# Kernel tuning notes

Hardware: AMD Instinct MI355X
Metric: run time of the kernel (lower is better)

The kernel has to match this reference:

```python
import jax, jax.numpy as jnp
import numpy as np

N = 50000          # nodes
E = 1600000        # edges (before self-loops)
DIN = 128
HEADS = (8, 8, 4)
FEATS = (16, 16, 16)
NEG_SLOPE = 0.2


def setup_inputs() -> dict:
    key = jax.random.key(0)
    ks = jax.random.split(key, 2 + 4 * 3)
    inp = {
        "X": jax.random.normal(ks[0], (N, DIN), dtype=jnp.float32),
        "A": jax.random.randint(ks[1], (2, E), 0, N, dtype=jnp.int32),
    }
    in_dims = [DIN, HEADS[0] * FEATS[0], HEADS[1] * FEATS[1]]
    k = 2
    for i, (h, f) in enumerate(zip(HEADS, FEATS)):
        din = in_dims[i]
        concat = i + 1 < len(HEADS)
        inp[f"W{i+1}"] = jax.random.normal(ks[k], (din, h * f), dtype=jnp.float32) / np.float32(np.sqrt(din)); k += 1
        inp[f"as{i+1}"] = jax.random.normal(ks[k], (h, f), dtype=jnp.float32) * 0.1; k += 1
        inp[f"ad{i+1}"] = jax.random.normal(ks[k], (h, f), dtype=jnp.float32) * 0.1; k += 1
        inp[f"b{i+1}"] = jnp.zeros((h * f if concat else f,), dtype=jnp.float32); k += 1
    return inp


def _gat_conv(x, src, dst, W, a_src, a_dst, b, concat):
    # PyG-style GATConv (eval mode, self-loops already in src/dst)
    H, F = a_src.shape
    h = (x @ W).reshape(-1, H, F)                     # [N, H, F]
    e = jax.nn.leaky_relu((h * a_src).sum(-1)[src] + (h * a_dst).sum(-1)[dst], NEG_SLOPE)  # [Etot, H]
    m = jax.ops.segment_max(e, dst, num_segments=N)   # segment softmax over dst neighborhoods
    ex = jnp.exp(e - m[dst])
    s = jax.ops.segment_sum(ex, dst, num_segments=N)
    alpha = ex / (s[dst] + 1e-16)                     # [Etot, H]
    out = jax.ops.segment_sum(h[src] * alpha[:, :, None], dst, num_segments=N)  # [N, H, F]
    out = out.reshape(N, H * F) if concat else out.mean(axis=1)
    return out + b


def reference(X, A, W1, as1, ad1, b1, W2, as2, ad2, b2, W3, as3, ad3, b3):
    loops = jnp.arange(N, dtype=A.dtype)              # GATConv default add_self_loops=True
    src = jnp.concatenate([A[0], loops])
    dst = jnp.concatenate([A[1], loops])
    x = jax.nn.relu(_gat_conv(X, src, dst, W1, as1, ad1, b1, True))
    x = jax.nn.relu(_gat_conv(x, src, dst, W2, as2, ad2, b2, True))
    return _gat_conv(x, src, dst, W3, as3, ad3, b3, False)
```

## Files before the change

kernel.cpp:

```cpp
#include <hip/hip_runtime.h>
#include <hip/hip_bf16.h>

#define NN 50000
#define EE 1600000
#define DIN 128

#define BKT_SHIFT 6
#define NB ((NN + 63) >> 6)
#define BSLACK 2688
#define CHUNK 4096

typedef _Float16 half_t;
typedef __attribute__((ext_vector_type(2))) _Float16 half2_t;
typedef __attribute__((ext_vector_type(4))) _Float16 half4_t;
typedef __attribute__((ext_vector_type(8))) _Float16 half8_t;
typedef __attribute__((ext_vector_type(4))) float float4_t;

__device__ __forceinline__ void split_write(half_t* __restrict__ bh, half_t* __restrict__ bl,
                                            int idx, float v) {
    half_t h = (half_t)v;
    bh[idx] = h;
    bl[idx] = (half_t)(v - (float)h);
}

__device__ __forceinline__ void build_bt(const float* __restrict__ W,
                                         const float* __restrict__ as,
                                         const float* __restrict__ ad,
                                         half_t* __restrict__ Bh, half_t* __restrict__ Bl,
                                         int elem, int NCOL, int H) {
    int r = elem >> 7, k = elem & 127;
    float v;
    if (r < NCOL) {
        v = W[k * NCOL + r];
    } else {
        int j = r - NCOL;
        v = 0.f;
        if (j < 8) {
            if (j < H) {
                float s = 0.f;
#pragma unroll
                for (int f = 0; f < 16; ++f) s += W[k * NCOL + j * 16 + f] * as[j * 16 + f];
                v = s;
            }
        } else {
            int hh = j - 8;
            if (hh < H) {
                float s = 0.f;
#pragma unroll
                for (int f = 0; f < 16; ++f) s += W[k * NCOL + hh * 16 + f] * ad[hh * 16 + f];
                v = s;
            }
        }
    }
    split_write(Bh, Bl, r * 128 + k, v);
}

#define T1 (144 * 128)
#define T3 (80 * 128)
__global__ __launch_bounds__(256) void prep_kernel(
    const float* __restrict__ W1, const float* __restrict__ W2, const float* __restrict__ W3,
    const float* __restrict__ as1, const float* __restrict__ ad1,
    const float* __restrict__ as2, const float* __restrict__ ad2,
    const float* __restrict__ as3, const float* __restrict__ ad3,
    half_t* __restrict__ B1h, half_t* __restrict__ B1l,
    half_t* __restrict__ B2h, half_t* __restrict__ B2l,
    half_t* __restrict__ B3h, half_t* __restrict__ B3l,
    int* __restrict__ gcursor) {
    int id = blockIdx.x * 256 + threadIdx.x;
    if (id < T1) {
        build_bt(W1, as1, ad1, B1h, B1l, id, 128, 8);
    } else if (id < 2 * T1) {
        build_bt(W2, as2, ad2, B2h, B2l, id - T1, 128, 8);
    } else if (id < 2 * T1 + T3) {
        build_bt(W3, as3, ad3, B3h, B3l, id - 2 * T1, 64, 4);
    } else {
        int i = id - (2 * T1 + T3);
        if (i < NB) gcursor[i] = 0;
    }
}

__global__ __launch_bounds__(256) void bin_kernel(const int* __restrict__ A,
                                                  int* __restrict__ gcursor,
                                                  int* __restrict__ binned, int e, int n) {
    __shared__ int lcount[NB];
    __shared__ int lbase[NB];
    int chunk0 = blockIdx.x * CHUNK;
    int cend = chunk0 + CHUNK;
    if (cend > e + n) cend = e + n;
    for (int i = threadIdx.x; i < NB; i += 256) lcount[i] = 0;
    __syncthreads();
    int sreg[16], dreg[16];
#pragma unroll
    for (int l = 0; l < 16; ++l) {
        int i = chunk0 + l * 256 + threadIdx.x;
        if (i < cend) {
            if (i < e) { sreg[l] = A[i]; dreg[l] = A[e + i]; }
            else       { sreg[l] = dreg[l] = i - e; }
            atomicAdd(&lcount[dreg[l] >> BKT_SHIFT], 1);
        } else {
            dreg[l] = -1;
        }
    }
    __syncthreads();
    for (int b = threadIdx.x; b < NB; b += 256) {
        int c = lcount[b];
        lbase[b] = c ? atomicAdd(&gcursor[b], c) : 0;
        lcount[b] = 0;
    }
    __syncthreads();
#pragma unroll
    for (int l = 0; l < 16; ++l) {
        if (dreg[l] >= 0) {
            int bkt = dreg[l] >> BKT_SHIFT;
            int pos = lbase[bkt] + atomicAdd(&lcount[bkt], 1);
            if (pos < BSLACK)
                binned[(size_t)bkt * BSLACK + pos] = (sreg[l] << 6) | (dreg[l] & 63);
        }
    }
}

__global__ __launch_bounds__(256) void fine_scatter(const int* __restrict__ binned,
                                                    const int* __restrict__ gcursor,
                                                    int* __restrict__ begE,
                                                    int* __restrict__ endE,
                                                    int* __restrict__ csr) {
    __shared__ int lc[64];
    __shared__ int scur[64];
    int b = blockIdx.x;
    int node0 = b << BKT_SHIFT;
    int cnt = gcursor[b];
    if (cnt > BSLACK) cnt = BSLACK;
    const int* bp = binned + (size_t)b * BSLACK;
    if (threadIdx.x < 64) lc[threadIdx.x] = 0;
    __syncthreads();
    for (int j = threadIdx.x; j < cnt; j += 256) atomicAdd(&lc[bp[j] & 63], 1);
    __syncthreads();
    if (threadIdx.x < 64) {
        int lane = threadIdx.x;
        int c = lc[lane];
        int v = c;
#pragma unroll
        for (int off = 1; off < 64; off <<= 1) {
            int u = __shfl_up(v, off, 64);
            if (lane >= off) v += u;
        }
        int begin = b * BSLACK + v - c;
        scur[lane] = begin;
        int node = node0 + lane;
        if (node < NN) {
            begE[node] = begin;
            endE[node] = begin + c;
        }
    }
    __syncthreads();
    for (int j = threadIdx.x; j < cnt; j += 256) {
        int v = bp[j];
        int pos = atomicAdd(&scur[v & 63], 1);
        csr[pos] = v >> 6;
    }
}

template <int NTC, int H, bool A32>
__global__ __launch_bounds__(256) void gemm_mfma(
    const float* __restrict__ X32,
    const half_t* __restrict__ Ah, const half_t* __restrict__ Al,
    const half_t* __restrict__ Bth, const half_t* __restrict__ Btl,
    half_t* __restrict__ C16, float* __restrict__ ss, float* __restrict__ ds, int M) {
    constexpr int NCOL = NTC * 16;
    constexpr int NR = NTC + 1;
    constexpr int NCHUNK = NR * 256;
    __shared__ __align__(16) half_t Bs[2][NR * 2048];
    int tid = threadIdx.x;
    int w = tid >> 6, lane = tid & 63;
    int m = lane & 15, q = lane >> 4;
    int row0 = blockIdx.x * 64 + w * 16;

    for (int P = tid; P < NCHUNK; P += 256) {
        int nt = P >> 8, k0 = (P >> 6) & 3, qq = (P >> 4) & 3, mm = P & 15;
        int src = (nt * 16 + mm) * 128 + qq * 8 + k0 * 32;
        *(half8_t*)&Bs[0][(size_t)P * 8] = *(const half8_t*)&Bth[src];
        *(half8_t*)&Bs[1][(size_t)P * 8] = *(const half8_t*)&Btl[src];
    }

    int ar = row0 + m;
    if (ar >= M) ar = M - 1;
    half8_t ahf[4], alf[4];
    if constexpr (A32) {
        const float* px = X32 + (size_t)ar * 128 + q * 8;
#pragma unroll
        for (int k0 = 0; k0 < 4; ++k0) {
            float4 u0 = *(const float4*)(px + k0 * 32);
            float4 u1 = *(const float4*)(px + k0 * 32 + 4);
            float uv[8] = {u0.x, u0.y, u0.z, u0.w, u1.x, u1.y, u1.z, u1.w};
#pragma unroll
            for (int j = 0; j < 8; ++j) {
                half_t h = (half_t)uv[j];
                ahf[k0][j] = h;
                alf[k0][j] = (half_t)(uv[j] - (float)h);
            }
        }
    } else {
        const half_t* pa = Ah + (size_t)ar * 128 + q * 8;
        const half_t* pl = Al + (size_t)ar * 128 + q * 8;
#pragma unroll
        for (int k0 = 0; k0 < 4; ++k0) {
            ahf[k0] = *(const half8_t*)(pa + k0 * 32);
            alf[k0] = *(const half8_t*)(pl + k0 * 32);
        }
    }

    __syncthreads();

    float4_t acc[NR];
#pragma unroll
    for (int nt = 0; nt < NR; ++nt) {
        acc[nt][0] = 0.f; acc[nt][1] = 0.f; acc[nt][2] = 0.f; acc[nt][3] = 0.f;
    }

#pragma unroll
    for (int nt = 0; nt < NR; ++nt) {
#pragma unroll
        for (int k0 = 0; k0 < 4; ++k0) {
            half8_t bh = *(const half8_t*)&Bs[0][(size_t)((nt * 4 + k0) * 64 + lane) * 8];
            half8_t bl = *(const half8_t*)&Bs[1][(size_t)((nt * 4 + k0) * 64 + lane) * 8];
            acc[nt] = __builtin_amdgcn_mfma_f32_16x16x32_f16(ahf[k0], bh, acc[nt], 0, 0, 0);
            acc[nt] = __builtin_amdgcn_mfma_f32_16x16x32_f16(ahf[k0], bl, acc[nt], 0, 0, 0);
            acc[nt] = __builtin_amdgcn_mfma_f32_16x16x32_f16(alf[k0], bh, acc[nt], 0, 0, 0);
        }
    }

#pragma unroll
    for (int r = 0; r < 4; ++r) {
        int grow = row0 + q * 4 + r;
        if (grow < M) {
            float v = acc[NTC][r];
            if (m < H) ss[(size_t)grow * H + m] = v;
            else if (m >= 8 && m < 8 + H) ds[(size_t)grow * H + (m - 8)] = v;
        }
    }

    __syncthreads();
    half_t* cs = (half_t*)Bs;
#pragma unroll
    for (int nt = 0; nt < NTC; ++nt)
#pragma unroll
        for (int r = 0; r < 4; ++r)
            cs[(size_t)(w * 16 + q * 4 + r) * NCOL + nt * 16 + m] = (half_t)acc[nt][r];
    constexpr int LPR = NCOL / 8;
    constexpr int RPP = 64 / LPR;
    constexpr int NP = 16 / RPP;
    int rid = lane / LPR, cid = lane % LPR;
#pragma unroll
    for (int p = 0; p < NP; ++p) {
        int r = p * RPP + rid;
        int grow = row0 + r;
        half8_t v = *(const half8_t*)&cs[(size_t)(w * 16 + r) * NCOL + cid * 8];
        if (grow < M) *(half8_t*)(C16 + (size_t)grow * NCOL + cid * 8) = v;
    }
}

template <int H, int F, bool MEAN, bool RELU>
__global__ __launch_bounds__(256) void aggregate_qw(
    const half_t* __restrict__ h, const float* __restrict__ ss, const float* __restrict__ dsc_arr,
    const int* __restrict__ csr, const int* __restrict__ begE, const int* __restrict__ endE,
    const float* __restrict__ bias, half_t* __restrict__ outh, half_t* __restrict__ outl,
    float* __restrict__ out, int n) {
    constexpr int HF = H * F;
    constexpr int FPL = HF / 16;
    int wave = blockIdx.x * (blockDim.x >> 6) + (threadIdx.x >> 6);
    int lane = threadIdx.x & 63;
    if (wave >= n) return;
    int q = lane >> 4, ql = lane & 15;
    int hf = ql * FPL;
    int hh = hf / F;
    float dsc = dsc_arr[wave * H + hh];
    int begin = begE[wave], end = endE[wave];

    float ssum = 0.f;
    float acc[FPL];
#pragma unroll
    for (int k = 0; k < FPL; ++k) acc[k] = 0.f;

    int j = begin + q;
    for (; j + 12 < end; j += 16) {
        int s0 = csr[j], s1 = csr[j + 4], s2 = csr[j + 8], s3 = csr[j + 12];
        float e0 = ss[s0 * H + hh], e1 = ss[s1 * H + hh];
        float e2 = ss[s2 * H + hh], e3 = ss[s3 * H + hh];
        const half_t* p0 = h + (size_t)s0 * HF + hf;
        const half_t* p1 = h + (size_t)s1 * HF + hf;
        const half_t* p2 = h + (size_t)s2 * HF + hf;
        const half_t* p3 = h + (size_t)s3 * HF + hf;
        e0 += dsc; e0 = (e0 > 0.f) ? e0 : 0.2f * e0;
        e1 += dsc; e1 = (e1 > 0.f) ? e1 : 0.2f * e1;
        e2 += dsc; e2 = (e2 > 0.f) ? e2 : 0.2f * e2;
        e3 += dsc; e3 = (e3 > 0.f) ? e3 : 0.2f * e3;
        float x0 = __expf(e0), x1 = __expf(e1), x2 = __expf(e2), x3 = __expf(e3);
        ssum += (x0 + x1) + (x2 + x3);
        if constexpr (FPL == 8) {
            half8_t t0 = *(const half8_t*)p0, t1 = *(const half8_t*)p1;
            half8_t t2 = *(const half8_t*)p2, t3 = *(const half8_t*)p3;
#pragma unroll
            for (int k = 0; k < 8; ++k) {
                acc[k] = fmaf(x0, (float)t0[k], acc[k]);
                acc[k] = fmaf(x1, (float)t1[k], acc[k]);
                acc[k] = fmaf(x2, (float)t2[k], acc[k]);
                acc[k] = fmaf(x3, (float)t3[k], acc[k]);
            }
        } else {
            half4_t t0 = *(const half4_t*)p0, t1 = *(const half4_t*)p1;
            half4_t t2 = *(const half4_t*)p2, t3 = *(const half4_t*)p3;
#pragma unroll
            for (int k = 0; k < 4; ++k) {
                acc[k] = fmaf(x0, (float)t0[k], acc[k]);
                acc[k] = fmaf(x1, (float)t1[k], acc[k]);
                acc[k] = fmaf(x2, (float)t2[k], acc[k]);
                acc[k] = fmaf(x3, (float)t3[k], acc[k]);
            }
        }
    }
    for (; j + 4 < end; j += 8) {
        int s0 = csr[j], s1 = csr[j + 4];
        float e0 = ss[s0 * H + hh], e1 = ss[s1 * H + hh];
        const half_t* p0 = h + (size_t)s0 * HF + hf;
        const half_t* p1 = h + (size_t)s1 * HF + hf;
        e0 += dsc; e0 = (e0 > 0.f) ? e0 : 0.2f * e0;
        e1 += dsc; e1 = (e1 > 0.f) ? e1 : 0.2f * e1;
        float x0 = __expf(e0), x1 = __expf(e1);
        ssum += x0 + x1;
        if constexpr (FPL == 8) {
            half8_t t0 = *(const half8_t*)p0, t1 = *(const half8_t*)p1;
#pragma unroll
            for (int k = 0; k < 8; ++k) {
                acc[k] = fmaf(x0, (float)t0[k], acc[k]);
                acc[k] = fmaf(x1, (float)t1[k], acc[k]);
            }
        } else {
            half4_t t0 = *(const half4_t*)p0, t1 = *(const half4_t*)p1;
#pragma unroll
            for (int k = 0; k < 4; ++k) {
                acc[k] = fmaf(x0, (float)t0[k], acc[k]);
                acc[k] = fmaf(x1, (float)t1[k], acc[k]);
            }
        }
    }
    for (; j < end; j += 4) {
        int s = csr[j];
        float e = ss[s * H + hh] + dsc;
        e = (e > 0.f) ? e : 0.2f * e;
        float x = __expf(e);
        ssum += x;
        const half_t* hp = h + (size_t)s * HF + hf;
        if constexpr (FPL == 8) {
            half8_t t = *(const half8_t*)hp;
#pragma unroll
            for (int k = 0; k < 8; ++k) acc[k] = fmaf(x, (float)t[k], acc[k]);
        } else {
            half4_t t = *(const half4_t*)hp;
#pragma unroll
            for (int k = 0; k < 4; ++k) acc[k] = fmaf(x, (float)t[k], acc[k]);
        }
    }

    ssum += __shfl_xor(ssum, 16, 64);
    ssum += __shfl_xor(ssum, 32, 64);
#pragma unroll
    for (int k = 0; k < FPL; ++k) {
        acc[k] += __shfl_xor(acc[k], 16, 64);
        acc[k] += __shfl_xor(acc[k], 32, 64);
    }

    float inv = 1.f / (ssum + 1e-16f);
    if constexpr (!MEAN) {
        if (lane < 32) {
            int k0 = (lane >> 4) * 4;
            int f = (lane & 15) * FPL + k0;
            float v[4];
#pragma unroll
            for (int i = 0; i < 4; ++i) {
                v[i] = acc[k0 + i] * inv + bias[f + i];
                if (RELU) v[i] = fmaxf(v[i], 0.f);
            }
            half4_t hh4, ll4;
#pragma unroll
            for (int i = 0; i < 4; ++i) {
                hh4[i] = (half_t)v[i];
                ll4[i] = (half_t)(v[i] - (float)hh4[i]);
            }
            *(half4_t*)(outh + (size_t)wave * HF + f) = hh4;
            *(half4_t*)(outl + (size_t)wave * HF + f) = ll4;
        }
    } else {
        float val[FPL];
#pragma unroll
        for (int k = 0; k < FPL; ++k) {
            val[k] = acc[k] * inv;
            val[k] += __shfl_xor(val[k], 4, 64);
            val[k] += __shfl_xor(val[k], 8, 64);
        }
        if (lane < 4) {
            float v0 = val[0] * 0.25f + bias[lane * 4 + 0];
            float v1 = val[1] * 0.25f + bias[lane * 4 + 1];
            float v2 = val[2] * 0.25f + bias[lane * 4 + 2];
            float v3 = val[3] * 0.25f + bias[lane * 4 + 3];
            *(float4*)(out + (size_t)wave * F + lane * 4) = make_float4(v0, v1, v2, v3);
        }
    }
}

extern "C" void kernel_launch(void* const* d_in, const int* in_sizes, int n_in,
                              void* d_out, int out_size, void* d_ws, size_t ws_size,
                              hipStream_t stream) {
    const float* X  = (const float*)d_in[0];
    const int*   A  = (const int*)d_in[1];
    const float* W1 = (const float*)d_in[2];
    const float* as1 = (const float*)d_in[3];
    const float* ad1 = (const float*)d_in[4];
    const float* b1  = (const float*)d_in[5];
    const float* W2 = (const float*)d_in[6];
    const float* as2 = (const float*)d_in[7];
    const float* ad2 = (const float*)d_in[8];
    const float* b2  = (const float*)d_in[9];
    const float* W3 = (const float*)d_in[10];
    const float* as3 = (const float*)d_in[11];
    const float* ad3 = (const float*)d_in[12];
    const float* b3  = (const float*)d_in[13];

    const int N = NN, E = EE;
    const int Etot = E + N;

    char* p = (char*)d_ws;
    auto take = [&](size_t bytes) {
        char* r = p;
        p += (bytes + 255) & ~(size_t)255;
        return (void*)r;
    };
    half_t* C16   = (half_t*)take((size_t)N * 128 * 2);
    half_t* Ph    = (half_t*)take((size_t)N * 128 * 2);
    half_t* Pl    = (half_t*)take((size_t)N * 128 * 2);
    float* ssb    = (float*)take((size_t)N * 8 * 4);
    float* dsb    = (float*)take((size_t)N * 8 * 4);
    int* begE     = (int*)take((size_t)N * 4);
    int* endE     = (int*)take((size_t)N * 4);
    int* gcursor  = (int*)take((size_t)NB * 4);
    int* csr      = (int*)take((size_t)NB * BSLACK * 4);
    half_t* B1h   = (half_t*)take(144 * 128 * 2);
    half_t* B1l   = (half_t*)take(144 * 128 * 2);
    half_t* B2h   = (half_t*)take(144 * 128 * 2);
    half_t* B2l   = (half_t*)take(144 * 128 * 2);
    half_t* B3h   = (half_t*)take(80 * 128 * 2);
    half_t* B3l   = (half_t*)take(80 * 128 * 2);
    int* binned   = (int*)Ph;

    const int prepTotal = 2 * T1 + T3 + NB;
    prep_kernel<<<(prepTotal + 255) / 256, 256, 0, stream>>>(
        W1, W2, W3, as1, ad1, as2, ad2, as3, ad3,
        B1h, B1l, B2h, B2l, B3h, B3l, gcursor);
    bin_kernel<<<(Etot + CHUNK - 1) / CHUNK, 256, 0, stream>>>(A, gcursor, binned, E, N);
    fine_scatter<<<NB, 256, 0, stream>>>(binned, gcursor, begE, endE, csr);

    const int gemmRows = (N + 63) / 64;
    const int aggBlocks = (N + 3) / 4;

    gemm_mfma<8, 8, true><<<gemmRows, 256, 0, stream>>>(X, nullptr, nullptr,
                                                        B1h, B1l, C16, ssb, dsb, N);
    aggregate_qw<8, 16, false, true>
        <<<aggBlocks, 256, 0, stream>>>(C16, ssb, dsb, csr, begE, endE, b1, Ph, Pl, nullptr, N);

    gemm_mfma<8, 8, false><<<gemmRows, 256, 0, stream>>>(nullptr, Ph, Pl,
                                                         B2h, B2l, C16, ssb, dsb, N);
    aggregate_qw<8, 16, false, true>
        <<<aggBlocks, 256, 0, stream>>>(C16, ssb, dsb, csr, begE, endE, b2, Ph, Pl, nullptr, N);

    gemm_mfma<4, 4, false><<<gemmRows, 256, 0, stream>>>(nullptr, Ph, Pl,
                                                         B3h, B3l, C16, ssb, dsb, N);
    aggregate_qw<4, 16, true, false>
        <<<aggBlocks, 256, 0, stream>>>(C16, ssb, dsb, csr, begE, endE, b3, nullptr, nullptr,
                                        (float*)d_out, N);
}
```

Before: 345.3 us.

## Slice 128-wide features into four 32-column planes for cache-local aggregation

Layers 1 and 2 now store GEMM outputs, source scores and the next layer's inputs in a sliced layout: four planes of 32 columns across all nodes. A new aggregate kernel assigns each block to one slice, so the random neighbour gathers touch a 3.2MB plane instead of the full 12.8MB feature array, aiming for better L2 locality. Each wave handles one destination node for one slice, with 8 edge groups of 8 lanes each. The trade-off is that edge indices and softmax exponentials are recomputed four times per node, and each gather is now only 8 bytes per lane.

Result: slower. 406.7 us (+17.8%).

```diff
diff --git a/kernel.cpp b/kernel.cpp
--- a/kernel.cpp
+++ b/kernel.cpp
@@ -160,7 +160,7 @@
     }
 }
 
-template <int NTC, int H, bool A32>
+template <int NTC, int H, int AMODE, bool CSL>
 __global__ __launch_bounds__(256) void gemm_mfma(
     const float* __restrict__ X32,
     const half_t* __restrict__ Ah, const half_t* __restrict__ Al,
@@ -185,7 +185,7 @@
     int ar = row0 + m;
     if (ar >= M) ar = M - 1;
     half8_t ahf[4], alf[4];
-    if constexpr (A32) {
+    if constexpr (AMODE == 0) {
         const float* px = X32 + (size_t)ar * 128 + q * 8;
 #pragma unroll
         for (int k0 = 0; k0 < 4; ++k0) {
@@ -200,12 +200,11 @@
             }
         }
     } else {
-        const half_t* pa = Ah + (size_t)ar * 128 + q * 8;
-        const half_t* pl = Al + (size_t)ar * 128 + q * 8;
 #pragma unroll
         for (int k0 = 0; k0 < 4; ++k0) {
-            ahf[k0] = *(const half8_t*)(pa + k0 * 32);
-            alf[k0] = *(const half8_t*)(pl + k0 * 32);
+            size_t base = ((size_t)k0 * M + ar) * 32 + q * 8;
+            ahf[k0] = *(const half8_t*)(Ah + base);
+            alf[k0] = *(const half8_t*)(Al + base);
         }
     }
 
@@ -234,8 +233,13 @@
         int grow = row0 + q * 4 + r;
         if (grow < M) {
             float v = acc[NTC][r];
-            if (m < H) ss[(size_t)grow * H + m] = v;
-            else if (m >= 8 && m < 8 + H) ds[(size_t)grow * H + (m - 8)] = v;
+            if constexpr (CSL) {
+                if (m < H) ss[(((size_t)(m >> 1)) * M + grow) * 2 + (m & 1)] = v;
+                else if (m >= 8 && m < 8 + H) ds[(size_t)grow * H + (m - 8)] = v;
+            } else {
+                if (m < H) ss[(size_t)grow * H + m] = v;
+                else if (m >= 8 && m < 8 + H) ds[(size_t)grow * H + (m - 8)] = v;
+            }
         }
     }
 
@@ -246,27 +250,115 @@
 #pragma unroll
         for (int r = 0; r < 4; ++r)
             cs[(size_t)(w * 16 + q * 4 + r) * NCOL + nt * 16 + m] = (half_t)acc[nt][r];
-    constexpr int LPR = NCOL / 8;
-    constexpr int RPP = 64 / LPR;
-    constexpr int NP = 16 / RPP;
-    int rid = lane / LPR, cid = lane % LPR;
-#pragma unroll
-    for (int p = 0; p < NP; ++p) {
-        int r = p * RPP + rid;
-        int grow = row0 + r;
-        half8_t v = *(const half8_t*)&cs[(size_t)(w * 16 + r) * NCOL + cid * 8];
-        if (grow < M) *(half8_t*)(C16 + (size_t)grow * NCOL + cid * 8) = v;
-    }
-}
-
-template <int H, int F, bool MEAN, bool RELU>
-__global__ __launch_bounds__(256) void aggregate_qw(
+    if constexpr (CSL) {
+        int sl = lane >> 4, rr = (lane >> 2) & 3, c = lane & 3;
+#pragma unroll
+        for (int pass = 0; pass < 4; ++pass) {
+            int r = pass * 4 + rr;
+            int grow = row0 + r;
+            half8_t v = *(const half8_t*)&cs[(size_t)(w * 16 + r) * NCOL + sl * 32 + c * 8];
+            if (grow < M) *(half8_t*)(C16 + ((size_t)sl * M + grow) * 32 + c * 8) = v;
+        }
+    } else {
+        constexpr int LPR = NCOL / 8;
+        constexpr int RPP = 64 / LPR;
+        constexpr int NP = 16 / RPP;
+        int rid = lane / LPR, cid = lane % LPR;
+#pragma unroll
+        for (int p = 0; p < NP; ++p) {
+            int r = p * RPP + rid;
+            int grow = row0 + r;
+            half8_t v = *(const half8_t*)&cs[(size_t)(w * 16 + r) * NCOL + cid * 8];
+            if (grow < M) *(half8_t*)(C16 + (size_t)grow * NCOL + cid * 8) = v;
+        }
+    }
+}
+
+template <bool RELU>
+__global__ __launch_bounds__(256) void aggregate_x(
+    const half_t* __restrict__ hS, const float* __restrict__ ssS,
+    const float* __restrict__ dsc_arr,
+    const int* __restrict__ csr, const int* __restrict__ begE, const int* __restrict__ endE,
+    const float* __restrict__ bias, half_t* __restrict__ outh, half_t* __restrict__ outl,
+    int n) {
+    constexpr int H = 8, SW = 32;
+    int b = blockIdx.x;
+    int s = b & 3;
+    int d = (b >> 2) * 4 + (threadIdx.x >> 6);
+    if (d >= n) return;
+    int lane = threadIdx.x & 63;
+    int g = lane >> 3, fl = lane & 7;
+    int f0 = s * SW + fl * 4;
+    int hh = f0 >> 4;
+    int sc = fl >> 2;
+    float dsc = dsc_arr[(size_t)d * H + hh];
+    const float* ssp = ssS + (size_t)s * n * 2;
+    const half_t* hp = hS + (size_t)s * n * SW;
+    int begin = begE[d], end = endE[d];
+
+    float ssum = 0.f, a0 = 0.f, a1 = 0.f, a2 = 0.f, a3 = 0.f;
+    int j = begin + g;
+    for (; j + 8 < end; j += 16) {
+        int u0 = csr[j], u1 = csr[j + 8];
+        float e0 = ssp[u0 * 2 + sc], e1 = ssp[u1 * 2 + sc];
+        half4_t t0 = *(const half4_t*)(hp + (size_t)u0 * SW + fl * 4);
+        half4_t t1 = *(const half4_t*)(hp + (size_t)u1 * SW + fl * 4);
+        e0 += dsc; e0 = (e0 > 0.f) ? e0 : 0.2f * e0;
+        e1 += dsc; e1 = (e1 > 0.f) ? e1 : 0.2f * e1;
+        float x0 = __expf(e0), x1 = __expf(e1);
+        ssum += x0 + x1;
+        a0 = fmaf(x0, (float)t0[0], a0); a0 = fmaf(x1, (float)t1[0], a0);
+        a1 = fmaf(x0, (float)t0[1], a1); a1 = fmaf(x1, (float)t1[1], a1);
+        a2 = fmaf(x0, (float)t0[2], a2); a2 = fmaf(x1, (float)t1[2], a2);
+        a3 = fmaf(x0, (float)t0[3], a3); a3 = fmaf(x1, (float)t1[3], a3);
+    }
+    for (; j < end; j += 8) {
+        int u = csr[j];
+        float e = ssp[u * 2 + sc] + dsc;
+        e = (e > 0.f) ? e : 0.2f * e;
+        half4_t t = *(const half4_t*)(hp + (size_t)u * SW + fl * 4);
+        float x = __expf(e);
+        ssum += x;
+        a0 = fmaf(x, (float)t[0], a0);
+        a1 = fmaf(x, (float)t[1], a1);
+        a2 = fmaf(x, (float)t[2], a2);
+        a3 = fmaf(x, (float)t[3], a3);
+    }
+
+    ssum += __shfl_xor(ssum, 8, 64);
+    ssum += __shfl_xor(ssum, 16, 64);
+    ssum += __shfl_xor(ssum, 32, 64);
+    a0 += __shfl_xor(a0, 8, 64); a0 += __shfl_xor(a0, 16, 64); a0 += __shfl_xor(a0, 32, 64);
+    a1 += __shfl_xor(a1, 8, 64); a1 += __shfl_xor(a1, 16, 64); a1 += __shfl_xor(a1, 32, 64);
+    a2 += __shfl_xor(a2, 8, 64); a2 += __shfl_xor(a2, 16, 64); a2 += __shfl_xor(a2, 32, 64);
+    a3 += __shfl_xor(a3, 8, 64); a3 += __shfl_xor(a3, 16, 64); a3 += __shfl_xor(a3, 32, 64);
+
+    if (lane < 8) {
+        float inv = 1.f / (ssum + 1e-16f);
+        float v0 = a0 * inv + bias[f0 + 0];
+        float v1 = a1 * inv + bias[f0 + 1];
+        float v2 = a2 * inv + bias[f0 + 2];
+        float v3 = a3 * inv + bias[f0 + 3];
+        if (RELU) {
+            v0 = fmaxf(v0, 0.f); v1 = fmaxf(v1, 0.f);
+            v2 = fmaxf(v2, 0.f); v3 = fmaxf(v3, 0.f);
+        }
+        half4_t hh4, ll4;
+        hh4[0] = (half_t)v0; ll4[0] = (half_t)(v0 - (float)hh4[0]);
+        hh4[1] = (half_t)v1; ll4[1] = (half_t)(v1 - (float)hh4[1]);
+        hh4[2] = (half_t)v2; ll4[2] = (half_t)(v2 - (float)hh4[2]);
+        hh4[3] = (half_t)v3; ll4[3] = (half_t)(v3 - (float)hh4[3]);
+        size_t o = ((size_t)s * n + d) * SW + fl * 4;
+        *(half4_t*)(outh + o) = hh4;
+        *(half4_t*)(outl + o) = ll4;
+    }
+}
+
+__global__ __launch_bounds__(256) void aggregate_l3(
     const half_t* __restrict__ h, const float* __restrict__ ss, const float* __restrict__ dsc_arr,
     const int* __restrict__ csr, const int* __restrict__ begE, const int* __restrict__ endE,
-    const float* __restrict__ bias, half_t* __restrict__ outh, half_t* __restrict__ outl,
-    float* __restrict__ out, int n) {
-    constexpr int HF = H * F;
-    constexpr int FPL = HF / 16;
+    const float* __restrict__ bias, float* __restrict__ out, int n) {
+    constexpr int H = 4, F = 16, HF = 64, FPL = 4;
     int wave = blockIdx.x * (blockDim.x >> 6) + (threadIdx.x >> 6);
     int lane = threadIdx.x & 63;
     if (wave >= n) return;
@@ -277,9 +369,7 @@
     int begin = begE[wave], end = endE[wave];
 
     float ssum = 0.f;
-    float acc[FPL];
-#pragma unroll
-    for (int k = 0; k < FPL; ++k) acc[k] = 0.f;
+    float acc[FPL] = {};
 
     int j = begin + q;
     for (; j + 12 < end; j += 16) {
@@ -296,51 +386,14 @@
         e3 += dsc; e3 = (e3 > 0.f) ? e3 : 0.2f * e3;
         float x0 = __expf(e0), x1 = __expf(e1), x2 = __expf(e2), x3 = __expf(e3);
         ssum += (x0 + x1) + (x2 + x3);
-        if constexpr (FPL == 8) {
-            half8_t t0 = *(const half8_t*)p0, t1 = *(const half8_t*)p1;
-            half8_t t2 = *(const half8_t*)p2, t3 = *(const half8_t*)p3;
-#pragma unroll
-            for (int k = 0; k < 8; ++k) {
-                acc[k] = fmaf(x0, (float)t0[k], acc[k]);
-                acc[k] = fmaf(x1, (float)t1[k], acc[k]);
-                acc[k] = fmaf(x2, (float)t2[k], acc[k]);
-                acc[k] = fmaf(x3, (float)t3[k], acc[k]);
-            }
-        } else {
-            half4_t t0 = *(const half4_t*)p0, t1 = *(const half4_t*)p1;
-            half4_t t2 = *(const half4_t*)p2, t3 = *(const half4_t*)p3;
-#pragma unroll
-            for (int k = 0; k < 4; ++k) {
-                acc[k] = fmaf(x0, (float)t0[k], acc[k]);
-                acc[k] = fmaf(x1, (float)t1[k], acc[k]);
-                acc[k] = fmaf(x2, (float)t2[k], acc[k]);
-                acc[k] = fmaf(x3, (float)t3[k], acc[k]);
-            }
-        }
-    }
-    for (; j + 4 < end; j += 8) {
-        int s0 = csr[j], s1 = csr[j + 4];
-        float e0 = ss[s0 * H + hh], e1 = ss[s1 * H + hh];
-        const half_t* p0 = h + (size_t)s0 * HF + hf;
-        const half_t* p1 = h + (size_t)s1 * HF + hf;
-        e0 += dsc; e0 = (e0 > 0.f) ? e0 : 0.2f * e0;
-        e1 += dsc; e1 = (e1 > 0.f) ? e1 : 0.2f * e1;
-        float x0 = __expf(e0), x1 = __expf(e1);
-        ssum += x0 + x1;
-        if constexpr (FPL == 8) {
-            half8_t t0 = *(const half8_t*)p0, t1 = *(const half8_t*)p1;
-#pragma unroll
-            for (int k = 0; k < 8; ++k) {
-                acc[k] = fmaf(x0, (float)t0[k], acc[k]);
-                acc[k] = fmaf(x1, (float)t1[k], acc[k]);
-            }
-        } else {
-            half4_t t0 = *(const half4_t*)p0, t1 = *(const half4_t*)p1;
-#pragma unroll
-            for (int k = 0; k < 4; ++k) {
-                acc[k] = fmaf(x0, (float)t0[k], acc[k]);
-                acc[k] = fmaf(x1, (float)t1[k], acc[k]);
-            }
+        half4_t t0 = *(const half4_t*)p0, t1 = *(const half4_t*)p1;
+        half4_t t2 = *(const half4_t*)p2, t3 = *(const half4_t*)p3;
+#pragma unroll
+        for (int k = 0; k < 4; ++k) {
+            acc[k] = fmaf(x0, (float)t0[k], acc[k]);
+            acc[k] = fmaf(x1, (float)t1[k], acc[k]);
+            acc[k] = fmaf(x2, (float)t2[k], acc[k]);
+            acc[k] = fmaf(x3, (float)t3[k], acc[k]);
         }
     }
     for (; j < end; j += 4) {
@@ -349,16 +402,9 @@
         e = (e > 0.f) ? e : 0.2f * e;
         float x = __expf(e);
         ssum += x;
-        const half_t* hp = h + (size_t)s * HF + hf;
-        if constexpr (FPL == 8) {
-            half8_t t = *(const half8_t*)hp;
-#pragma unroll
-            for (int k = 0; k < 8; ++k) acc[k] = fmaf(x, (float)t[k], acc[k]);
-        } else {
-            half4_t t = *(const half4_t*)hp;
-#pragma unroll
-            for (int k = 0; k < 4; ++k) acc[k] = fmaf(x, (float)t[k], acc[k]);
-        }
+        half4_t t = *(const half4_t*)(h + (size_t)s * HF + hf);
+#pragma unroll
+        for (int k = 0; k < 4; ++k) acc[k] = fmaf(x, (float)t[k], acc[k]);
     }
 
     ssum += __shfl_xor(ssum, 16, 64);
@@ -370,40 +416,19 @@
     }
 
     float inv = 1.f / (ssum + 1e-16f);
-    if constexpr (!MEAN) {
-        if (lane < 32) {
-            int k0 = (lane >> 4) * 4;
-            int f = (lane & 15) * FPL + k0;
-            float v[4];
-#pragma unroll
-            for (int i = 0; i < 4; ++i) {
-                v[i] = acc[k0 + i] * inv + bias[f + i];
-                if (RELU) v[i] = fmaxf(v[i], 0.f);
-            }
-            half4_t hh4, ll4;
-#pragma unroll
-            for (int i = 0; i < 4; ++i) {
-                hh4[i] = (half_t)v[i];
-                ll4[i] = (half_t)(v[i] - (float)hh4[i]);
-            }
-            *(half4_t*)(outh + (size_t)wave * HF + f) = hh4;
-            *(half4_t*)(outl + (size_t)wave * HF + f) = ll4;
-        }
-    } else {
-        float val[FPL];
-#pragma unroll
-        for (int k = 0; k < FPL; ++k) {
-            val[k] = acc[k] * inv;
-            val[k] += __shfl_xor(val[k], 4, 64);
-            val[k] += __shfl_xor(val[k], 8, 64);
-        }
-        if (lane < 4) {
-            float v0 = val[0] * 0.25f + bias[lane * 4 + 0];
-            float v1 = val[1] * 0.25f + bias[lane * 4 + 1];
-            float v2 = val[2] * 0.25f + bias[lane * 4 + 2];
-            float v3 = val[3] * 0.25f + bias[lane * 4 + 3];
-            *(float4*)(out + (size_t)wave * F + lane * 4) = make_float4(v0, v1, v2, v3);
-        }
+    float val[FPL];
+#pragma unroll
+    for (int k = 0; k < FPL; ++k) {
+        val[k] = acc[k] * inv;
+        val[k] += __shfl_xor(val[k], 4, 64);
+        val[k] += __shfl_xor(val[k], 8, 64);
+    }
+    if (lane < 4) {
+        float v0 = val[0] * 0.25f + bias[lane * 4 + 0];
+        float v1 = val[1] * 0.25f + bias[lane * 4 + 1];
+        float v2 = val[2] * 0.25f + bias[lane * 4 + 2];
+        float v3 = val[3] * 0.25f + bias[lane * 4 + 3];
+        *(float4*)(out + (size_t)wave * F + lane * 4) = make_float4(v0, v1, v2, v3);
     }
 }
 
@@ -459,21 +484,21 @@
     fine_scatter<<<NB, 256, 0, stream>>>(binned, gcursor, begE, endE, csr);
 
     const int gemmRows = (N + 63) / 64;
+    const int aggXBlocks = ((N + 3) / 4) * 4;
     const int aggBlocks = (N + 3) / 4;
 
-    gemm_mfma<8, 8, true><<<gemmRows, 256, 0, stream>>>(X, nullptr, nullptr,
-                                                        B1h, B1l, C16, ssb, dsb, N);
-    aggregate_qw<8, 16, false, true>
-        <<<aggBlocks, 256, 0, stream>>>(C16, ssb, dsb, csr, begE, endE, b1, Ph, Pl, nullptr, N);
-
-    gemm_mfma<8, 8, false><<<gemmRows, 256, 0, stream>>>(nullptr, Ph, Pl,
-                                                         B2h, B2l, C16, ssb, dsb, N);
-    aggregate_qw<8, 16, false, true>
-        <<<aggBlocks, 256, 0, stream>>>(C16, ssb, dsb, csr, begE, endE, b2, Ph, Pl, nullptr, N);
-
-    gemm_mfma<4, 4, false><<<gemmRows, 256, 0, stream>>>(nullptr, Ph, Pl,
-                                                         B3h, B3l, C16, ssb, dsb, N);
-    aggregate_qw<4, 16, true, false>
-        <<<aggBlocks, 256, 0, stream>>>(C16, ssb, dsb, csr, begE, endE, b3, nullptr, nullptr,
-                                        (float*)d_out, N);
-}
+    gemm_mfma<8, 8, 0, true><<<gemmRows, 256, 0, stream>>>(X, nullptr, nullptr,
+                                                           B1h, B1l, C16, ssb, dsb, N);
+    aggregate_x<true><<<aggXBlocks, 256, 0, stream>>>(
+        C16, ssb, dsb, csr, begE, endE, b1, Ph, Pl, N);
+
+    gemm_mfma<8, 8, 1, true><<<gemmRows, 256, 0, stream>>>(nullptr, Ph, Pl,
+                                                           B2h, B2l, C16, ssb, dsb, N);
+    aggregate_x<true><<<aggXBlocks, 256, 0, stream>>>(
+        C16, ssb, dsb, csr, begE, endE, b2, Ph, Pl, N);
+
+    gemm_mfma<4, 4, 1, false><<<gemmRows, 256, 0, stream>>>(nullptr, Ph, Pl,
+                                                            B3h, B3l, C16, ssb, dsb, N);
+    aggregate_l3<<<aggBlocks, 256, 0, stream>>>(
+        C16, ssb, dsb, csr, begE, endE, b3, (float*)d_out, N);
+}
```
